# Kernel tuning notes

Measured on AMD Instinct MI355X. Metric: run time of the kernel, lower is better.

The kernel has to match this reference:

```python
import jax, jax.numpy as jnp
import numpy as np
from jax import lax

B, N, C = 2, 4096, 8
MAX_DET = 100
SCORE_THR = 0.01
NMS_THR = 0.5
NEG = -1e30  # sentinel for masked scores


def setup_inputs() -> dict:
    key = jax.random.key(0)
    k1, k2, k3, k4, k5 = jax.random.split(key, 5)
    # valid xyxy boxes: centers in [0,512), extents in [2,66)
    ctr = jax.random.uniform(k1, (B, N, 2), dtype=jnp.float32) * 512.0
    wh = jax.random.uniform(k2, (B, N, 2), dtype=jnp.float32) * 64.0 + 2.0
    boxes = jnp.concatenate([ctr - wh / 2, ctr + wh / 2], axis=-1)  # [B,N,4]
    classification = jax.random.uniform(k3, (B, N, C), dtype=jnp.float32)
    rotation = jax.random.normal(k4, (B, N, 3), dtype=jnp.float32)
    translation = jax.random.normal(k5, (B, N, 3), dtype=jnp.float32)
    return {"boxes": boxes, "classification": classification,
            "rotation": rotation, "translation": translation}


def _pairwise_iou(b):
    # b: [N,4] xyxy, torchvision convention (no +1)
    x1, y1, x2, y2 = b[:, 0], b[:, 1], b[:, 2], b[:, 3]
    area = (x2 - x1) * (y2 - y1)
    ix1 = jnp.maximum(x1[:, None], x1[None, :])
    iy1 = jnp.maximum(y1[:, None], y1[None, :])
    ix2 = jnp.minimum(x2[:, None], x2[None, :])
    iy2 = jnp.minimum(y2[:, None], y2[None, :])
    inter = jnp.clip(ix2 - ix1, 0.0) * jnp.clip(iy2 - iy1, 0.0)
    union = area[:, None] + area[None, :] - inter
    return inter / jnp.maximum(union, 1e-9)


def _nms_keep(boxes, scores, valid):
    # greedy NMS matching torchvision.ops.nms on the `valid` subset.
    order = jnp.argsort(-jnp.where(valid, scores, NEG))  # score-descending
    iou = _pairwise_iou(boxes[order])  # [N,N]
    idx = jnp.arange(N)
    keep0 = valid[order]

    def body(i, keep):
        sup = keep[i] & (iou[i] > NMS_THR) & (idx > i)
        return keep & ~sup

    keep_sorted = lax.fori_loop(0, N, body, keep0)
    return jnp.zeros(N, bool).at[order].set(keep_sorted)


def _filter_image(boxes, cls, rot, trans):
    # boxes [N,4], cls [N,C], rot [N,3], trans [N,3]
    def per_class(scores):
        valid = scores > SCORE_THR
        keep = _nms_keep(boxes, scores, valid)
        return jnp.where(keep, scores, NEG)

    masked = jax.vmap(per_class, in_axes=1)(cls)  # [C,N]
    topv, topi = lax.top_k(masked.reshape(-1), MAX_DET)
    labels = topi // N
    anchors = topi % N
    ok = topv > NEG / 2
    okc = ok[:, None]
    boxes_o = jnp.where(okc, boxes[anchors], -1.0)
    scores_o = jnp.where(ok, topv, -1.0)
    labels_o = jnp.where(ok, labels, -1)
    rot_o = jnp.where(okc, rot[anchors], -1.0)
    trans_o = jnp.where(okc, trans[anchors], -1.0)
    return boxes_o, scores_o, labels_o, rot_o, trans_o


def reference(boxes, classification, rotation, translation):
    return jax.vmap(_filter_image)(boxes, classification, rotation, translation)
```

## Files before the change

kernel.cpp:

```cpp
#include <hip/hip_runtime.h>
#include <stdint.h>

#define B_ 2
#define N_ 4096
#define C_ 8
#define MAXDET 100
#define SCORE_THR 0.01f
#define NMS_THR 0.5f
#define NEGV -1e30f

typedef unsigned long long u64;

__device__ __forceinline__ unsigned mono_key(float f) {
    unsigned u = __float_as_uint(f);
    return (u & 0x80000000u) ? ~u : (u | 0x80000000u);
}
__device__ __forceinline__ float mono_dec(unsigned m) {
    return (m & 0x80000000u) ? __uint_as_float(m ^ 0x80000000u)
                             : __uint_as_float(~m);
}
__device__ __forceinline__ bool iou_gt_half(float inter, float uni) {
    return (inter + inter - uni) > uni * 0x1p-25f;
}
__device__ __forceinline__ void wave_fence() {
    asm volatile("s_waitcnt lgkmcnt(0)" ::: "memory");
}

__device__ __forceinline__ void ce_shfl(u64 &e0, u64 &e1, int tid, int size,
                                        int stride, bool desc) {
    const int m = stride >> 1;
    bool d = (((2 * tid) & size) == 0) ? desc : !desc;
    bool lower = (tid & m) == 0;
    u64 p0 = __shfl_xor(e0, m, 64);
    u64 p1 = __shfl_xor(e1, m, 64);
    bool takeMax = (d == lower);
    e0 = takeMax ? (e0 > p0 ? e0 : p0) : (e0 < p0 ? e0 : p0);
    e1 = takeMax ? (e1 > p1 ? e1 : p1) : (e1 < p1 ? e1 : p1);
}
__device__ __forceinline__ void ce_intra(u64 &e0, u64 &e1, int tid, int size,
                                         bool desc) {
    bool d = (((2 * tid) & size) == 0) ? desc : !desc;
    if ((e0 < e1) == d) { u64 t = e0; e0 = e1; e1 = t; }
}

__global__ __launch_bounds__(512) void sortA_kernel(
    const float* __restrict__ cls,
    u64* __restrict__ keys)
{
    __shared__ u64 k[1024];
    const int q = blockIdx.x;
    const int bc = blockIdx.y;
    const int b = bc >> 3, c = bc & 7;
    const int tid = threadIdx.x;
    const bool desc = ((q & 1) == 0);

    u64 e0, e1;
    {
        int i0 = q * 1024 + 2 * tid;
        float s0 = cls[((size_t)b * N_ + i0) * C_ + c];
        float s1 = cls[((size_t)b * N_ + i0 + 1) * C_ + c];
        float f0 = (s0 > SCORE_THR) ? s0 : NEGV;
        float f1 = (s1 > SCORE_THR) ? s1 : NEGV;
        e0 = ((u64)mono_key(f0) << 32) | (unsigned)(~i0);
        e1 = ((u64)mono_key(f1) << 32) | (unsigned)(~(i0 + 1));
    }

    #pragma unroll
    for (int size = 2; size <= 128; size <<= 1) {
        #pragma unroll
        for (int stride = size >> 1; stride >= 2; stride >>= 1)
            ce_shfl(e0, e1, tid, size, stride, desc);
        ce_intra(e0, e1, tid, size, desc);
    }
    #pragma unroll
    for (int size = 256; size <= 1024; size <<= 1) {
        k[2 * tid] = e0; k[2 * tid + 1] = e1;
        __syncthreads();
        for (int stride = size >> 1; stride >= 128; stride >>= 1) {
            int pos = 2 * tid - (tid & (stride - 1));
            int par = pos + stride;
            bool d = ((pos & size) == 0) ? desc : !desc;
            u64 a = k[pos], bb = k[par];
            if ((a < bb) == d) { k[pos] = bb; k[par] = a; }
            __syncthreads();
        }
        e0 = k[2 * tid]; e1 = k[2 * tid + 1];
        #pragma unroll
        for (int stride = 64; stride >= 2; stride >>= 1)
            ce_shfl(e0, e1, tid, size, stride, desc);
        ce_intra(e0, e1, tid, size, desc);
    }

    ulonglong2 v; v.x = e0; v.y = e1;
    *(ulonglong2*)&keys[(size_t)bc * N_ + q * 1024 + 2 * tid] = v;
}

__global__ __launch_bounds__(512) void fused_kernel(
    const u64* __restrict__ keys,
    const float* __restrict__ boxes,
    u64* __restrict__ cand)
{
    __shared__ u64 m[4096];
    __shared__ float4 sb192[192];
    __shared__ float  sa192[192];
    __shared__ u64 cm[576];
    __shared__ float4 sbx[64];
    __shared__ u64 shJ[64];
    __shared__ int s_fin;

    const int bc = blockIdx.x;
    const int b = bc >> 3, cls = bc & 7;
    const int tid = threadIdx.x;
    const int lane = tid & 63;
    const int wave = tid >> 6;
    const size_t kbase = (size_t)bc * N_;
    const float4* boxes4 = (const float4*)boxes;

    u64 e0, e1;
    {
        int i = 2 * tid;
        int qq = i >> 8;
        int off = qq * 1024 + ((qq & 1) ? 768 : 0) + (i & 255);
        ulonglong2 v = *(const ulonglong2*)&keys[kbase + off];
        e0 = v.x; e1 = v.y;
    }

    #pragma unroll
    for (int size = 512; size <= 1024; size <<= 1) {
        m[2 * tid] = e0; m[2 * tid + 1] = e1;
        __syncthreads();
        for (int stride = size >> 1; stride >= 128; stride >>= 1) {
            int pos = 2 * tid - (tid & (stride - 1));
            int par = pos + stride;
            bool d = ((pos & size) == 0);
            u64 a = m[pos], bb = m[par];
            if ((a < bb) == d) { m[pos] = bb; m[par] = a; }
            __syncthreads();
        }
        e0 = m[2 * tid]; e1 = m[2 * tid + 1];
        #pragma unroll
        for (int stride = 64; stride >= 2; stride >>= 1)
            ce_shfl(e0, e1, tid, size, stride, true);
        ce_intra(e0, e1, tid, size, true);
    }
    m[2 * tid] = e0; m[2 * tid + 1] = e1;
    __syncthreads();

    if (tid < 192) {
        int orig = (int)(~(unsigned)m[tid]);
        float4 bx = boxes4[(size_t)b * N_ + orig];
        sb192[tid] = bx;
        sa192[tid] = (bx.z - bx.x) * (bx.w - bx.y);
    }
    __syncthreads();

    {
        int s = tid, r = -1, w = 0;
        if (s < 192)      { r = s;       w = 2; }
        else if (s < 320) { r = s - 192; w = 1; }
        else if (s < 384) { r = s - 320; w = 0; }
        if (r >= 0) {
            float4 bi = sb192[r];
            float aarea = sa192[r];
            u64 bits = 0ull;
            #pragma unroll 8
            for (int t = 0; t < 64; t++) {
                float4 bj = sb192[w * 64 + t];
                float barea = sa192[w * 64 + t];
                float ix1 = fmaxf(bi.x, bj.x);
                float iy1 = fmaxf(bi.y, bj.y);
                float ix2 = fminf(bi.z, bj.z);
                float iy2 = fminf(bi.w, bj.w);
                float inter = fmaxf(ix2 - ix1, 0.0f) * fmaxf(iy2 - iy1, 0.0f);
                float uni = fmaxf(aarea + barea - inter, 1e-9f);
                if (iou_gt_half(inter, uni)) bits |= (1ull << t);
            }
            if (w == (r >> 6)) bits &= ~((2ull << (r & 63)) - 1ull);
            cm[r * 3 + w] = bits;
        } else {
            int z = s - 384;
            cm[(64 + z) * 3 + 0] = 0ull;
            if (z < 64)
                cm[(128 + z) * 3 + 1] = 0ull;
        }
    }
    __syncthreads();

    if (wave == 0) {
        u64 remv = 0ull;
        int cc = 0;
        bool fin = false;
        for (int c = 0; c < 3; c++) {
            int p = c * 64 + lane;
            u64 key = m[p];
            float sc = mono_dec((unsigned)(key >> 32));
            u64 validb = __ballot(sc > -1e29f);
            if (validb == 0ull) { fin = true; break; }

            u64 ivr = cm[(c * 64 + lane) * 3 + c];
            u64 curw = __shfl(remv, c, 64);
            u64 kept = 0ull;
            for (int t = 0; t < 64; t++) {
                u64 iv = __shfl(ivr, t, 64);
                u64 bit = 1ull << t;
                if (!(curw & bit) && (validb & bit)) { kept |= bit; curw |= iv; }
            }

            if ((kept >> lane) & 1ull) {
                int rank = cc + __popcll(kept & ((1ull << lane) - 1ull));
                if (rank < 128) {
                    int orig = (int)(~(unsigned)key);
                    unsigned flat = (unsigned)(cls * N_ + orig);
                    cand[bc * 128 + rank] =
                        ((u64)mono_key(sc) << 32) | (unsigned)(~flat);
                }
            }
            cc += __popcll(kept);
            if (cc >= 128) { fin = true; break; }

            if (lane < 3) {
                u64 acc = 0ull;
                for (int t = 0; t < 64; t++)
                    if ((kept >> t) & 1ull) acc |= cm[(c * 64 + t) * 3 + lane];
                remv |= acc;
            }
        }
        if (fin) {
            int filled = cc < 128 ? cc : 128;
            for (int s = lane; s < 128; s += 64)
                if (s >= filled) cand[bc * 128 + s] = 0ull;
        }
        if (lane == 0) s_fin = fin ? 1 : 0;
    }
    __syncthreads();
    if (s_fin) return;

    for (int i = tid; i < 4096; i += 512) m[i] = keys[kbase + i];
    __syncthreads();
    for (int size = 2048; size <= 4096; size <<= 1) {
        for (int stride = size >> 1; stride > 0; stride >>= 1) {
            for (int t = tid; t < 2048; t += 512) {
                int pos = 2 * t - (t & (stride - 1));
                int par = pos + stride;
                bool d = ((pos & size) == 0);
                u64 a = m[pos], bb = m[par];
                if ((a < bb) == d) { m[pos] = bb; m[par] = a; }
            }
            __syncthreads();
        }
    }
    if (wave != 0) return;

    {
        u64 remv = 0ull;
        int cc = 0;
        for (int c = 0; c < 64; c++) {
            int p = c * 64 + lane;
            u64 key = m[p];
            float sc = mono_dec((unsigned)(key >> 32));
            u64 validb = __ballot(sc > -1e29f);
            if (validb == 0ull) break;

            int orig = (int)(~(unsigned)key);
            float4 bl = boxes4[(size_t)b * N_ + orig];
            sbx[lane] = bl;
            wave_fence();
            float al = (bl.z - bl.x) * (bl.w - bl.y);

            u64 intra = 0ull;
            for (int t = 0; t < 64; t++) {
                float4 bj = sbx[t];
                float ab = (bj.z - bj.x) * (bj.w - bj.y);
                float ix1 = fmaxf(bl.x, bj.x);
                float iy1 = fmaxf(bl.y, bj.y);
                float ix2 = fminf(bl.z, bj.z);
                float iy2 = fminf(bl.w, bj.w);
                float inter = fmaxf(ix2 - ix1, 0.0f) * fmaxf(iy2 - iy1, 0.0f);
                float uni = fmaxf(al + ab - inter, 1e-9f);
                if (t > lane && iou_gt_half(inter, uni)) intra |= (1ull << t);
            }
            shJ[lane] = intra;
            wave_fence();

            u64 curw = __shfl(remv, c, 64);
            u64 kept = 0ull;
            for (int t = 0; t < 64; t++) {
                u64 iv = shJ[t];
                u64 bit = 1ull << t;
                if (!(curw & bit) && (validb & bit)) { kept |= bit; curw |= iv; }
            }

            if ((kept >> lane) & 1ull) {
                int rank = cc + __popcll(kept & ((1ull << lane) - 1ull));
                if (rank < 128) {
                    unsigned flat = (unsigned)(cls * N_ + orig);
                    cand[bc * 128 + rank] =
                        ((u64)mono_key(sc) << 32) | (unsigned)(~flat);
                }
            }
            cc += __popcll(kept);
            if (cc >= 128) break;

            if (lane > c) {
                u64 accw = 0ull;
                for (int u = 0; u < 64; u++) {
                    int pj = lane * 64 + u;
                    int oj = (int)(~(unsigned)m[pj]);
                    float4 bj = boxes4[(size_t)b * N_ + oj];
                    float ab = (bj.z - bj.x) * (bj.w - bj.y);
                    bool sup = false;
                    for (int tt = 0; tt < 64; tt++) {
                        if (!((kept >> tt) & 1ull)) continue;
                        float4 br = sbx[tt];
                        float ar = (br.z - br.x) * (br.w - br.y);
                        float ix1 = fmaxf(br.x, bj.x);
                        float iy1 = fmaxf(br.y, bj.y);
                        float ix2 = fminf(br.z, bj.z);
                        float iy2 = fminf(br.w, bj.w);
                        float inter = fmaxf(ix2 - ix1, 0.0f) * fmaxf(iy2 - iy1, 0.0f);
                        float uni = fmaxf(ar + ab - inter, 1e-9f);
                        if (iou_gt_half(inter, uni)) { sup = true; break; }
                    }
                    if (sup) accw |= (1ull << u);
                }
                remv |= accw;
            }
            wave_fence();
        }
        int filled = cc < 128 ? cc : 128;
        for (int s = lane; s < 128; s += 64)
            if (s >= filled) cand[bc * 128 + s] = 0ull;
    }
}

__global__ __launch_bounds__(1024) void merge_kernel(
    const u64* __restrict__ cand,
    const float* __restrict__ boxes,
    const float* __restrict__ rot,
    const float* __restrict__ trans,
    float* __restrict__ out)
{
    __shared__ u64 sk[1024];
    const int b = blockIdx.x;
    const int tid = threadIdx.x;
    const int c = tid >> 7, s = tid & 127;

    int src = (c & 1) ? (c * 128 + (127 - s)) : tid;
    sk[tid] = cand[(size_t)b * 1024 + src];

    for (int size = 256; size <= 1024; size <<= 1) {
        for (int stride = size >> 1; stride > 0; stride >>= 1) {
            __syncthreads();
            int partner = tid ^ stride;
            if (partner > tid) {
                bool desc = ((tid & size) == 0);
                u64 a = sk[tid], bb = sk[partner];
                if ((a < bb) == desc) { sk[tid] = bb; sk[partner] = a; }
            }
        }
    }
    __syncthreads();

    if (tid < MAXDET) {
        u64 key = sk[tid];
        float score = mono_dec((unsigned)(key >> 32));
        bool ok = score > (NEGV * 0.5f);
        unsigned flat = (~(unsigned)key) & 32767u;
        int cc = flat >> 12;
        int n = flat & (N_ - 1);

        float* obox = out;
        float* oscr = out + 800;
        float* olab = out + 1000;
        float* orot = out + 1200;
        float* otrn = out + 1800;

        #pragma unroll
        for (int d = 0; d < 4; d++)
            obox[b * 400 + tid * 4 + d] =
                ok ? boxes[((size_t)b * N_ + n) * 4 + d] : -1.0f;
        oscr[b * MAXDET + tid] = ok ? score : -1.0f;
        olab[b * MAXDET + tid] = ok ? (float)cc : -1.0f;
        #pragma unroll
        for (int d = 0; d < 3; d++) {
            orot[b * 300 + tid * 3 + d] =
                ok ? rot[((size_t)b * N_ + n) * 3 + d] : -1.0f;
            otrn[b * 300 + tid * 3 + d] =
                ok ? trans[((size_t)b * N_ + n) * 3 + d] : -1.0f;
        }
    }
}

extern "C" void kernel_launch(void* const* d_in, const int* in_sizes, int n_in,
                              void* d_out, int out_size, void* d_ws, size_t ws_size,
                              hipStream_t stream) {
    const float* boxes = (const float*)d_in[0];
    const float* cls   = (const float*)d_in[1];
    const float* rot   = (const float*)d_in[2];
    const float* trans = (const float*)d_in[3];
    float* out = (float*)d_out;

    char* w = (char*)d_ws;
    u64* keys = (u64*)w;   w += (size_t)B_ * C_ * N_ * sizeof(u64);
    u64* cand = (u64*)w;   w += (size_t)B_ * C_ * 128 * sizeof(u64);

    sortA_kernel<<<dim3(4, B_ * C_), 512, 0, stream>>>(cls, keys);
    fused_kernel<<<B_ * C_, 512, 0, stream>>>(keys, boxes, cand);
    merge_kernel<<<B_, 1024, 0, stream>>>(cand, boxes, rot, trans, out);
}
```

Measured before the change: 96.92 us.

## Fuse per-quarter score sort into the NMS kernel with register-resident bitonic sort

```diff
diff --git a/kernel.cpp b/kernel.cpp
--- a/kernel.cpp
+++ b/kernel.cpp
@@ -24,6 +24,9 @@
 }
 __device__ __forceinline__ void wave_fence() {
     asm volatile("s_waitcnt lgkmcnt(0)" ::: "memory");
+}
+__device__ __forceinline__ void ce(u64 &a, u64 &b, bool d) {
+    if ((a < b) == d) { u64 t = a; a = b; b = t; }
 }
 
 __device__ __forceinline__ void ce_shfl(u64 &e0, u64 &e1, int tid, int size,
@@ -42,65 +45,32 @@
     bool d = (((2 * tid) & size) == 0) ? desc : !desc;
     if ((e0 < e1) == d) { u64 t = e0; e0 = e1; e1 = t; }
 }
-
-__global__ __launch_bounds__(512) void sortA_kernel(
+__device__ __forceinline__ void merge_hybrid(u64 &e0, u64 &e1, u64* k, int tid,
+                                             int size, bool desc) {
+    k[2 * tid] = e0; k[2 * tid + 1] = e1;
+    __syncthreads();
+    for (int stride = size >> 1; stride >= 128; stride >>= 1) {
+        int pos = 2 * tid - (tid & (stride - 1));
+        int par = pos + stride;
+        bool d = ((pos & size) == 0) ? desc : !desc;
+        u64 a = k[pos], bb = k[par];
+        if ((a < bb) == d) { k[pos] = bb; k[par] = a; }
+        __syncthreads();
+    }
+    e0 = k[2 * tid]; e1 = k[2 * tid + 1];
+    #pragma unroll
+    for (int stride = 64; stride >= 2; stride >>= 1)
+        ce_shfl(e0, e1, tid, size, stride, desc);
+    ce_intra(e0, e1, tid, size, desc);
+}
+
+__global__ __launch_bounds__(512) void bigfused_kernel(
     const float* __restrict__ cls,
-    u64* __restrict__ keys)
-{
-    __shared__ u64 k[1024];
-    const int q = blockIdx.x;
-    const int bc = blockIdx.y;
-    const int b = bc >> 3, c = bc & 7;
-    const int tid = threadIdx.x;
-    const bool desc = ((q & 1) == 0);
-
-    u64 e0, e1;
-    {
-        int i0 = q * 1024 + 2 * tid;
-        float s0 = cls[((size_t)b * N_ + i0) * C_ + c];
-        float s1 = cls[((size_t)b * N_ + i0 + 1) * C_ + c];
-        float f0 = (s0 > SCORE_THR) ? s0 : NEGV;
-        float f1 = (s1 > SCORE_THR) ? s1 : NEGV;
-        e0 = ((u64)mono_key(f0) << 32) | (unsigned)(~i0);
-        e1 = ((u64)mono_key(f1) << 32) | (unsigned)(~(i0 + 1));
-    }
-
-    #pragma unroll
-    for (int size = 2; size <= 128; size <<= 1) {
-        #pragma unroll
-        for (int stride = size >> 1; stride >= 2; stride >>= 1)
-            ce_shfl(e0, e1, tid, size, stride, desc);
-        ce_intra(e0, e1, tid, size, desc);
-    }
-    #pragma unroll
-    for (int size = 256; size <= 1024; size <<= 1) {
-        k[2 * tid] = e0; k[2 * tid + 1] = e1;
-        __syncthreads();
-        for (int stride = size >> 1; stride >= 128; stride >>= 1) {
-            int pos = 2 * tid - (tid & (stride - 1));
-            int par = pos + stride;
-            bool d = ((pos & size) == 0) ? desc : !desc;
-            u64 a = k[pos], bb = k[par];
-            if ((a < bb) == d) { k[pos] = bb; k[par] = a; }
-            __syncthreads();
-        }
-        e0 = k[2 * tid]; e1 = k[2 * tid + 1];
-        #pragma unroll
-        for (int stride = 64; stride >= 2; stride >>= 1)
-            ce_shfl(e0, e1, tid, size, stride, desc);
-        ce_intra(e0, e1, tid, size, desc);
-    }
-
-    ulonglong2 v; v.x = e0; v.y = e1;
-    *(ulonglong2*)&keys[(size_t)bc * N_ + q * 1024 + 2 * tid] = v;
-}
-
-__global__ __launch_bounds__(512) void fused_kernel(
-    const u64* __restrict__ keys,
     const float* __restrict__ boxes,
     u64* __restrict__ cand)
 {
     __shared__ u64 m[4096];
+    __shared__ u64 scr[1024];
     __shared__ float4 sb192[192];
     __shared__ float  sa192[192];
     __shared__ u64 cm[576];
@@ -109,45 +79,90 @@
     __shared__ int s_fin;
 
     const int bc = blockIdx.x;
-    const int b = bc >> 3, cls = bc & 7;
+    const int b = bc >> 3, cls_id = bc & 7;
     const int tid = threadIdx.x;
     const int lane = tid & 63;
     const int wave = tid >> 6;
-    const size_t kbase = (size_t)bc * N_;
     const float4* boxes4 = (const float4*)boxes;
 
-    u64 e0, e1;
     {
+        const int q = tid >> 7;
+        const int lt = tid & 127;
+        const bool desc = ((q & 1) == 0);
+        u64* mm = &m[q * 1024];
+
+        u64 k[8];
+        #pragma unroll
+        for (int j = 0; j < 8; j++) {
+            int i = q * 1024 + lt * 8 + j;
+            float s = cls[((size_t)b * N_ + i) * C_ + cls_id];
+            float f = (s > SCORE_THR) ? s : NEGV;
+            k[j] = ((u64)mono_key(f) << 32) | (unsigned)(~i);
+        }
+
+        ce(k[0], k[1], desc ); ce(k[2], k[3], !desc);
+        ce(k[4], k[5], desc ); ce(k[6], k[7], !desc);
+        ce(k[0], k[2], desc ); ce(k[1], k[3], desc );
+        ce(k[4], k[6], !desc); ce(k[5], k[7], !desc);
+        ce(k[0], k[1], desc ); ce(k[2], k[3], desc );
+        ce(k[4], k[5], !desc); ce(k[6], k[7], !desc);
+
+        for (int size = 8; size <= 1024; size <<= 1) {
+            const bool dthr = ((lt & (size >> 3)) == 0) ? desc : !desc;
+            int stride = size >> 1;
+            if (stride >= 512) {
+                #pragma unroll
+                for (int j = 0; j < 8; j++) mm[lt * 8 + j] = k[j];
+                __syncthreads();
+                {
+                    const u64* pp = &mm[(lt ^ 64) * 8];
+                    const bool takeMax = (dthr == (lt < 64));
+                    #pragma unroll
+                    for (int j = 0; j < 8; j++) {
+                        u64 p = pp[j];
+                        k[j] = takeMax ? (k[j] > p ? k[j] : p)
+                                       : (k[j] < p ? k[j] : p);
+                    }
+                }
+                __syncthreads();
+                stride = 256;
+            }
+            for (; stride >= 8; stride >>= 1) {
+                const int ls = stride >> 3;
+                const bool takeMax = (dthr == ((lt & ls) == 0));
+                #pragma unroll
+                for (int j = 0; j < 8; j++) {
+                    u64 p = __shfl_xor(k[j], ls, 64);
+                    k[j] = takeMax ? (k[j] > p ? k[j] : p)
+                                   : (k[j] < p ? k[j] : p);
+                }
+            }
+            ce(k[0], k[4], dthr); ce(k[1], k[5], dthr);
+            ce(k[2], k[6], dthr); ce(k[3], k[7], dthr);
+            ce(k[0], k[2], dthr); ce(k[1], k[3], dthr);
+            ce(k[4], k[6], dthr); ce(k[5], k[7], dthr);
+            ce(k[0], k[1], dthr); ce(k[2], k[3], dthr);
+            ce(k[4], k[5], dthr); ce(k[6], k[7], dthr);
+        }
+        #pragma unroll
+        for (int j = 0; j < 8; j++) mm[lt * 8 + j] = k[j];
+    }
+    __syncthreads();
+
+    {
+        u64 e0, e1;
         int i = 2 * tid;
         int qq = i >> 8;
         int off = qq * 1024 + ((qq & 1) ? 768 : 0) + (i & 255);
-        ulonglong2 v = *(const ulonglong2*)&keys[kbase + off];
-        e0 = v.x; e1 = v.y;
-    }
-
-    #pragma unroll
-    for (int size = 512; size <= 1024; size <<= 1) {
-        m[2 * tid] = e0; m[2 * tid + 1] = e1;
-        __syncthreads();
-        for (int stride = size >> 1; stride >= 128; stride >>= 1) {
-            int pos = 2 * tid - (tid & (stride - 1));
-            int par = pos + stride;
-            bool d = ((pos & size) == 0);
-            u64 a = m[pos], bb = m[par];
-            if ((a < bb) == d) { m[pos] = bb; m[par] = a; }
-            __syncthreads();
-        }
-        e0 = m[2 * tid]; e1 = m[2 * tid + 1];
-        #pragma unroll
-        for (int stride = 64; stride >= 2; stride >>= 1)
-            ce_shfl(e0, e1, tid, size, stride, true);
-        ce_intra(e0, e1, tid, size, true);
-    }
-    m[2 * tid] = e0; m[2 * tid + 1] = e1;
+        e0 = m[off]; e1 = m[off + 1];
+        merge_hybrid(e0, e1, scr, tid, 512, true);
+        merge_hybrid(e0, e1, scr, tid, 1024, true);
+        scr[2 * tid] = e0; scr[2 * tid + 1] = e1;
+    }
     __syncthreads();
 
     if (tid < 192) {
-        int orig = (int)(~(unsigned)m[tid]);
+        int orig = (int)(~(unsigned)scr[tid]);
         float4 bx = boxes4[(size_t)b * N_ + orig];
         sb192[tid] = bx;
         sa192[tid] = (bx.z - bx.x) * (bx.w - bx.y);
@@ -192,7 +207,7 @@
         bool fin = false;
         for (int c = 0; c < 3; c++) {
             int p = c * 64 + lane;
-            u64 key = m[p];
+            u64 key = scr[p];
             float sc = mono_dec((unsigned)(key >> 32));
             u64 validb = __ballot(sc > -1e29f);
             if (validb == 0ull) { fin = true; break; }
@@ -210,7 +225,7 @@
                 int rank = cc + __popcll(kept & ((1ull << lane) - 1ull));
                 if (rank < 128) {
                     int orig = (int)(~(unsigned)key);
-                    unsigned flat = (unsigned)(cls * N_ + orig);
+                    unsigned flat = (unsigned)(cls_id * N_ + orig);
                     cand[bc * 128 + rank] =
                         ((u64)mono_key(sc) << 32) | (unsigned)(~flat);
                 }
@@ -235,8 +250,6 @@
     __syncthreads();
     if (s_fin) return;
 
-    for (int i = tid; i < 4096; i += 512) m[i] = keys[kbase + i];
-    __syncthreads();
     for (int size = 2048; size <= 4096; size <<= 1) {
         for (int stride = size >> 1; stride > 0; stride >>= 1) {
             for (int t = tid; t < 2048; t += 512) {
@@ -293,7 +306,7 @@
             if ((kept >> lane) & 1ull) {
                 int rank = cc + __popcll(kept & ((1ull << lane) - 1ull));
                 if (rank < 128) {
-                    unsigned flat = (unsigned)(cls * N_ + orig);
+                    unsigned flat = (unsigned)(cls_id * N_ + orig);
                     cand[bc * 128 + rank] =
                         ((u64)mono_key(sc) << 32) | (unsigned)(~flat);
                 }
@@ -400,11 +413,8 @@
     const float* trans = (const float*)d_in[3];
     float* out = (float*)d_out;
 
-    char* w = (char*)d_ws;
-    u64* keys = (u64*)w;   w += (size_t)B_ * C_ * N_ * sizeof(u64);
-    u64* cand = (u64*)w;   w += (size_t)B_ * C_ * 128 * sizeof(u64);
-
-    sortA_kernel<<<dim3(4, B_ * C_), 512, 0, stream>>>(cls, keys);
-    fused_kernel<<<B_ * C_, 512, 0, stream>>>(keys, boxes, cand);
+    u64* cand = (u64*)d_ws;
+
+    bigfused_kernel<<<B_ * C_, 512, 0, stream>>>(cls, boxes, cand);
     merge_kernel<<<B_, 1024, 0, stream>>>(cand, boxes, rot, trans, out);
 }
```

New measurement: 104.7 us. 8.0% more time.
